# Optimization experiments

Measured on AMD Instinct MI355X. Metric: run time of the kernel, lower is better.

Reference implementation:

```python
import jax, jax.numpy as jnp
import numpy as np

D = 768
NH = 8
HD = D // NH
LAT = 64


def layernorm(x, g, b, eps=1e-5):
    mu = x.mean(-1, keepdims=True)
    var = ((x - mu) ** 2).mean(-1, keepdims=True)
    return (x - mu) * jax.lax.rsqrt(var + eps) * g + b


def mha(q, k, v, qw, qb, kw, kb, vw, vb, ow, ob):
    # torch nn.MultiheadAttention (batch_first): Linear is x @ W.T + b
    B, Lq, _ = q.shape
    qh = (q @ qw.T + qb).reshape(B, Lq, NH, HD)
    kh = (k @ kw.T + kb).reshape(B, -1, NH, HD)
    vh = (v @ vw.T + vb).reshape(B, -1, NH, HD)
    s = jnp.einsum('bqhd,bkhd->bhqk', qh, kh) * (1.0 / np.sqrt(HD))
    a = jax.nn.softmax(s, axis=-1)
    o = jnp.einsum('bhqk,bkhd->bqhd', a, vh).reshape(B, Lq, D)
    return o @ ow.T + ob


def setup_inputs() -> dict:
    key = jax.random.key(0)
    ks = jax.random.split(key, 16)
    w = lambda k, shape: (jax.random.normal(k, shape, jnp.float32) * 0.02)
    inp = {
        'frames': jax.random.normal(ks[0], (4, 4, 8, 3, 224, 224), jnp.float32),
        'pe_w': w(ks[1], (D, 3, 14, 14)), 'pe_b': jnp.zeros((D,), jnp.float32),
        'latents': jax.random.normal(ks[2], (LAT, D), jnp.float32),
        'ca_qw': w(ks[3], (D, D)), 'ca_qb': jnp.zeros((D,), jnp.float32),
        'ca_kw': w(ks[4], (D, D)), 'ca_kb': jnp.zeros((D,), jnp.float32),
        'ca_vw': w(ks[5], (D, D)), 'ca_vb': jnp.zeros((D,), jnp.float32),
        'ca_ow': w(ks[6], (D, D)), 'ca_ob': jnp.zeros((D,), jnp.float32),
        'nq_g': jnp.ones((D,), jnp.float32), 'nq_b': jnp.zeros((D,), jnp.float32),
        'nkv_g': jnp.ones((D,), jnp.float32), 'nkv_b': jnp.zeros((D,), jnp.float32),
        'no_g': jnp.ones((D,), jnp.float32), 'no_b': jnp.zeros((D,), jnp.float32),
        'm1_w': w(ks[7], (4 * D, D)), 'm1_b': jnp.zeros((4 * D,), jnp.float32),
        'm2_w': w(ks[8], (D, 4 * D)), 'm2_b': jnp.zeros((D,), jnp.float32),
        'sa_qw': w(ks[9], (D, D)), 'sa_qb': jnp.zeros((D,), jnp.float32),
        'sa_kw': w(ks[10], (D, D)), 'sa_kb': jnp.zeros((D,), jnp.float32),
        'sa_vw': w(ks[11], (D, D)), 'sa_vb': jnp.zeros((D,), jnp.float32),
        'sa_ow': w(ks[12], (D, D)), 'sa_ob': jnp.zeros((D,), jnp.float32),
        'f1_w': w(ks[13], (2 * D, D)), 'f1_b': jnp.zeros((2 * D,), jnp.float32),
        'f2_w': w(ks[14], (D, 2 * D)), 'f2_b': jnp.zeros((D,), jnp.float32),
        'n1_g': jnp.ones((D,), jnp.float32), 'n1_b': jnp.zeros((D,), jnp.float32),
        'n2_g': jnp.ones((D,), jnp.float32), 'n2_b': jnp.zeros((D,), jnp.float32),
    }
    return inp


def reference(frames, pe_w, pe_b, latents, ca_qw, ca_qb, ca_kw, ca_kb, ca_vw, ca_vb,
              ca_ow, ca_ob, nq_g, nq_b, nkv_g, nkv_b, no_g, no_b, m1_w, m1_b, m2_w, m2_b,
              sa_qw, sa_qb, sa_kw, sa_kb, sa_vw, sa_vb, sa_ow, sa_ob, f1_w, f1_b,
              f2_w, f2_b, n1_g, n1_b, n2_g, n2_b):
    B, S, T, C, H, W = frames.shape
    # --- patch embed (Conv2d k=14 s=14), batched over all seconds & frames ---
    f = frames.reshape(B * S * T, C, H, W)
    p = jax.lax.conv_general_dilated(
        f, pe_w, window_strides=(14, 14), padding='VALID',
        dimension_numbers=('NCHW', 'OIHW', 'NCHW')) + pe_b[None, :, None, None]
    npatch = p.shape[2] * p.shape[3]  # 256 patches per frame
    p = p.reshape(B * S * T, D, npatch).transpose(0, 2, 1)  # [BST, P, D]
    kv = p.reshape(B * S, T * npatch, D)  # per-second patch tokens
    # --- Perceiver second tokenizer (loop over seconds == batched over B*S) ---
    q = jnp.broadcast_to(latents[None], (B * S, LAT, D))
    out = mha(layernorm(q, nq_g, nq_b), layernorm(kv, nkv_g, nkv_b), kv,
              ca_qw, ca_qb, ca_kw, ca_kb, ca_vw, ca_vb, ca_ow, ca_ob)
    h = layernorm(out, no_g, no_b)
    tok = out + (jax.nn.gelu(h @ m1_w.T + m1_b) @ m2_w.T + m2_b)
    # concat second tokens along time
    x = tok.reshape(B, S * LAT, D)
    # --- temporal_agg: TransformerEncoderLayer (post-norm, relu, eval mode) ---
    attn = mha(x, x, x, sa_qw, sa_qb, sa_kw, sa_kb, sa_vw, sa_vb, sa_ow, sa_ob)
    x = layernorm(x + attn, n1_g, n1_b)
    ff = jax.nn.relu(x @ f1_w.T + f1_b) @ f2_w.T + f2_b
    x = layernorm(x + ff, n2_g, n2_b)
    return x
```

## Files before the change

kernel.cpp:

```cpp
#include <hip/hip_runtime.h>
#include <hip/hip_bf16.h>
#include <math.h>

typedef __hip_bfloat16 bf16;
typedef __attribute__((ext_vector_type(8))) short short8;
typedef __attribute__((ext_vector_type(4))) short short4v;
typedef __attribute__((ext_vector_type(4))) float f32x4;

__device__ __forceinline__ void gload16(const bf16* g, bf16* l) {
  __builtin_amdgcn_global_load_lds((const __attribute__((address_space(1))) void*)(g),
                                   (__attribute__((address_space(3))) void*)(l), 16, 0, 0);
}
__device__ __forceinline__ float bfu2f(unsigned short u) {
  union { unsigned u; float f; } c; c.u = ((unsigned)u) << 16; return c.f;
}
__device__ __forceinline__ short bf2s(float v) {
  union { bf16 h; short s; } c; c.h = __float2bfloat16(v); return c.s;
}
__device__ __forceinline__ short4v packbf4(f32x4 v) {
  short4v o;
  o[0] = bf2s(v[0]); o[1] = bf2s(v[1]); o[2] = bf2s(v[2]); o[3] = bf2s(v[3]);
  return o;
}

struct Seg { const float* src; bf16* dst; int rows, sc, dc; const float* scale; };
struct Segs { Seg s[13]; };

__global__ __launch_bounds__(256) void prepack_kernel(Segs segs) {
  Seg sg = segs.s[blockIdx.y];
  long long total = (long long)sg.rows * sg.dc;
  for (long long idx = (long long)blockIdx.x * 256 + threadIdx.x; idx < total;
       idx += (long long)gridDim.x * 256) {
    int r = (int)(idx / sg.dc), c = (int)(idx % sg.dc);
    float v = (c < sg.sc) ? sg.src[(long long)r * sg.sc + c] : 0.f;
    if (sg.scale && c < sg.sc) v *= sg.scale[c];
    sg.dst[idx] = __float2bfloat16(v);
  }
}

__global__ __launch_bounds__(256) void concat3_kernel(const float* __restrict__ a,
                                                      const float* __restrict__ b,
                                                      const float* __restrict__ c,
                                                      float* __restrict__ o) {
  int i = blockIdx.x * 256 + threadIdx.x;
  if (i < 2304)
    o[i] = i < 768 ? a[i] : (i < 1536 ? b[i - 768] : c[i - 1536]);
}

__global__ __launch_bounds__(256) void s12_kernel(const float* __restrict__ kw,
                                                  const float* __restrict__ g,
                                                  const float* __restrict__ b,
                                                  const float* __restrict__ kb,
                                                  float* __restrict__ s1,
                                                  float* __restrict__ s2) {
  int j = blockIdx.x;
  int tid = threadIdx.x;
  const float* wr_ = kw + (size_t)j * 768;
  float a = 0.f, c = 0.f;
  #pragma unroll
  for (int i = 0; i < 3; ++i) {
    int d = tid + i * 256;
    float wv = wr_[d];
    a += wv * g[d];
    c += wv * b[d];
  }
  __shared__ float red[16];
  for (int off = 32; off; off >>= 1) { a += __shfl_down(a, off); c += __shfl_down(c, off); }
  int w = tid >> 6;
  if ((tid & 63) == 0) { red[w] = a; red[8 + w] = c; }
  __syncthreads();
  if (tid == 0) {
    s1[j] = red[0] + red[1] + red[2] + red[3];
    s2[j] = red[8] + red[9] + red[10] + red[11] + kb[j];
  }
}

__global__ __launch_bounds__(256) void rowstats_kernel(const bf16* __restrict__ x,
                                                       float* __restrict__ mu,
                                                       float* __restrict__ rs) {
  int row = blockIdx.x * 4 + (threadIdx.x >> 6);
  int lane = threadIdx.x & 63;
  const unsigned short* p = (const unsigned short*)(x + (size_t)row * 768);
  float s = 0.f, sq = 0.f;
  #pragma unroll
  for (int i = 0; i < 3; ++i) {
    ushort4 v = *(const ushort4*)(p + lane * 4 + i * 256);
    float f0 = bfu2f(v.x), f1 = bfu2f(v.y), f2 = bfu2f(v.z), f3 = bfu2f(v.w);
    s += f0 + f1 + f2 + f3;
    sq += f0 * f0 + f1 * f1 + f2 * f2 + f3 * f3;
  }
  for (int off = 32; off; off >>= 1) { s += __shfl_down(s, off); sq += __shfl_down(sq, off); }
  if (lane == 0) {
    float m = s * (1.f / 768.f);
    float var = sq * (1.f / 768.f) - m * m;
    mu[row] = m;
    rs[row] = rsqrtf(var + 1e-5f);
  }
}

__global__ __launch_bounds__(256) void im2col_kernel(const float* __restrict__ frames,
                                                     bf16* __restrict__ out) {
  unsigned idx8 = blockIdx.x * 256u + threadIdx.x;
  unsigned m = idx8 / 76u;
  unsigned k0 = (idx8 % 76u) * 8u;
  unsigned n = m >> 8;
  unsigned p = m & 255u;
  unsigned py = p >> 4, px = p & 15u;
  const float* fb = frames + ((size_t)n * 3u) * 224u * 224u + (size_t)py * 14u * 224u +
                    px * 14u;
  short8 o;
  #pragma unroll
  for (int e = 0; e < 8; ++e) {
    unsigned k = k0 + e;
    float v = 0.f;
    if (k < 588u) {
      unsigned c = k / 196u, r = k % 196u;
      unsigned i = r / 14u, j = r % 14u;
      v = fb[((size_t)c * 224u + i) * 224u + j];
    }
    o[e] = bf2s(v);
  }
  *(short8*)(out + (size_t)m * 608u + k0) = o;
}

__global__ __launch_bounds__(256) void ln_kernel(const float* __restrict__ inF,
                                                 const bf16* __restrict__ inB,
                                                 const float* __restrict__ g,
                                                 const float* __restrict__ b,
                                                 float* __restrict__ outF,
                                                 bf16* __restrict__ outB,
                                                 int validRows) {
  int row = blockIdx.x;
  int tid = threadIdx.x;
  __shared__ float red[8];
  size_t base = (size_t)row * 768;
  if (row >= validRows) {
    for (int i = 0; i < 3; ++i) {
      int c = tid + i * 256;
      if (outB) outB[base + c] = __float2bfloat16(0.f);
      if (outF) outF[base + c] = 0.f;
    }
    return;
  }
  float x[3];
  for (int i = 0; i < 3; ++i) {
    int c = tid + i * 256;
    x[i] = inF ? inF[base + c] : __bfloat162float(inB[base + c]);
  }
  float s = x[0] + x[1] + x[2];
  float sq = x[0] * x[0] + x[1] * x[1] + x[2] * x[2];
  for (int off = 32; off; off >>= 1) {
    s += __shfl_down(s, off);
    sq += __shfl_down(sq, off);
  }
  int w = tid >> 6;
  if ((tid & 63) == 0) { red[w] = s; red[4 + w] = sq; }
  __syncthreads();
  if (tid == 0) {
    red[0] = red[0] + red[1] + red[2] + red[3];
    red[4] = red[4] + red[5] + red[6] + red[7];
  }
  __syncthreads();
  float mean = red[0] * (1.f / 768.f);
  float var = red[4] * (1.f / 768.f) - mean * mean;
  float rs = rsqrtf(var + 1e-5f);
  for (int i = 0; i < 3; ++i) {
    int c = tid + i * 256;
    float y = (x[i] - mean) * rs * g[c] + b[c];
    if (outF) outF[base + c] = y;
    if (outB) outB[base + c] = __float2bfloat16(y);
  }
}

__global__ __launch_bounds__(256) void gemm_bf16(
    const bf16* __restrict__ A, const bf16* __restrict__ Bw,
    const float* __restrict__ bias, const float* __restrict__ resid,
    float* __restrict__ outF, bf16* __restrict__ outB,
    int M, int N, int K, int act,
    const float* __restrict__ rowMu, const float* __restrict__ rowRs,
    const float* __restrict__ s1, const float* __restrict__ s2,
    bf16* __restrict__ outB2) {
  __shared__ __align__(16) bf16 As[2][4096];
  __shared__ __align__(16) bf16 Bs[2][4096];
  int tid = threadIdx.x;
  int nwg = gridDim.x * gridDim.y;
  int orig = blockIdx.y * gridDim.x + blockIdx.x;
  int xcd = orig & 7, loc = orig >> 3;
  int qq = nwg >> 3, rr = nwg & 7;
  int swz = (xcd < rr) ? (xcd * (qq + 1) + loc) : (rr * (qq + 1) + (xcd - rr) * qq + loc);
  int m0 = (swz / gridDim.x) * 128, n0 = (swz % gridDim.x) * 128;

  int lane = tid & 63, w = tid >> 6;
  int wr = w >> 1, wc = w & 1;
  int l15 = lane & 15, lq = lane >> 4;
  const bf16* Abase = A + (size_t)m0 * K + w * 8;
  const bf16* Bbase = Bw + (size_t)n0 * K + w * 8;
  f32x4 acc[4][4] = {};

  int nt = K >> 5;
  #pragma unroll
  for (int i = 0; i < 2; ++i) {
    int r = i * 64 + lane;
    gload16(Abase + (size_t)r * K, &As[0][(w * 2 + i) * 512]);
    gload16(Bbase + (size_t)r * K, &Bs[0][(w * 2 + i) * 512]);
  }
  for (int t = 0; t < nt; ++t) {
    int cur = t & 1;
    if (t + 1 < nt) {
      int kt = (t + 1) << 5;
      #pragma unroll
      for (int i = 0; i < 2; ++i) {
        int r = i * 64 + lane;
        gload16(Abase + (size_t)r * K + kt, &As[cur ^ 1][(w * 2 + i) * 512]);
        gload16(Bbase + (size_t)r * K + kt, &Bs[cur ^ 1][(w * 2 + i) * 512]);
      }
      asm volatile("s_waitcnt vmcnt(4)" ::: "memory");
    } else {
      asm volatile("s_waitcnt vmcnt(0)" ::: "memory");
    }
    __builtin_amdgcn_s_barrier();
    asm volatile("" ::: "memory");
    const bf16* Ab = &As[cur][lq * 1024];
    const bf16* Bb = &Bs[cur][lq * 1024];
    short8 af[4], bfr[4];
    #pragma unroll
    for (int mi = 0; mi < 4; ++mi)
      af[mi] = *(const short8*)(Ab + (wr * 64 + mi * 16 + l15) * 8);
    #pragma unroll
    for (int ni = 0; ni < 4; ++ni)
      bfr[ni] = *(const short8*)(Bb + (wc * 64 + ni * 16 + l15) * 8);
    __builtin_amdgcn_s_setprio(1);
    #pragma unroll
    for (int mi = 0; mi < 4; ++mi)
      #pragma unroll
      for (int ni = 0; ni < 4; ++ni)
        acc[mi][ni] = __builtin_amdgcn_mfma_f32_16x16x32_bf16(bfr[ni], af[mi],
                                                              acc[mi][ni], 0, 0, 0);
    __builtin_amdgcn_s_setprio(0);
    asm volatile("" ::: "memory");
    __builtin_amdgcn_s_barrier();
  }

  if (act == 3) {
    #pragma unroll
    for (int ni = 0; ni < 4; ++ni) {
      int c0 = n0 + wc * 64 + ni * 16 + lq * 4;
      if (c0 < 768) {
        f32x4 bv = *(const f32x4*)(bias + c0);
        #pragma unroll
        for (int mi = 0; mi < 4; ++mi) {
          int row = m0 + wr * 64 + mi * 16 + l15;
          f32x4 v = acc[mi][ni] + bv;
          *(short4v*)(outB + (size_t)row * 768 + c0) = packbf4(v);
        }
      } else {
        int ck = c0 - 768;
        f32x4 a1 = *(const f32x4*)(s1 + ck);
        f32x4 a2 = *(const f32x4*)(s2 + ck);
        #pragma unroll
        for (int mi = 0; mi < 4; ++mi) {
          int row = m0 + wr * 64 + mi * 16 + l15;
          float rs_ = rowRs[row], mu_ = rowMu[row];
          f32x4 v;
          #pragma unroll
          for (int j = 0; j < 4; ++j) v[j] = rs_ * (acc[mi][ni][j] - mu_ * a1[j]) + a2[j];
          *(short4v*)(outB2 + (size_t)row * 768 + ck) = packbf4(v);
        }
      }
    }
    return;
  }

  #pragma unroll
  for (int ni = 0; ni < 4; ++ni) {
    int c0 = n0 + wc * 64 + ni * 16 + lq * 4;
    f32x4 bv = {};
    if (bias) bv = *(const f32x4*)(bias + c0);
    #pragma unroll
    for (int mi = 0; mi < 4; ++mi) {
      int row = m0 + wr * 64 + mi * 16 + l15;
      f32x4 v = acc[mi][ni] + bv;
      if (act == 1) {
        #pragma unroll
        for (int j = 0; j < 4; ++j) {
          float x = v[j];
          v[j] = 0.5f * x * (1.f + tanhf(0.79788456080286535f * (x + 0.044715f * x * x * x)));
        }
      } else if (act == 2) {
        #pragma unroll
        for (int j = 0; j < 4; ++j) v[j] = fmaxf(v[j], 0.f);
      }
      size_t idx = (size_t)row * N + c0;
      if (resid) v += *(const f32x4*)(resid + idx);
      if (outF) *(f32x4*)(outF + idx) = v;
      if (outB) *(short4v*)(outB + idx) = packbf4(v);
    }
  }
}

__global__ __launch_bounds__(256) void flash_kernel(
    const bf16* __restrict__ Q, const bf16* __restrict__ Kp,
    const bf16* __restrict__ V, bf16* __restrict__ O,
    int Lk, int qRPB, int kRPB, int oRPB, int ld) {
  const float scale = 0.10206207261596575f;
  __shared__ bf16 Vt[96 * 72];
  __shared__ bf16 Ps[4 * 16 * 72];
  int tid = threadIdx.x, lane = tid & 63, w = tid >> 6;
  int l15 = lane & 15, lq = lane >> 4;
  int b = blockIdx.z, h = blockIdx.y, qt = blockIdx.x;
  int qbase = b * qRPB + qt * 64 + w * 16;
  int kbase = b * kRPB;
  int obase = b * oRPB + qt * 64 + w * 16;
  int ch = h * 96;

  short8 aQ[3];
  #pragma unroll
  for (int kd = 0; kd < 3; ++kd)
    aQ[kd] = *(const short8*)(Q + (size_t)(qbase + l15) * ld + ch + kd * 32 + lq * 8);

  f32x4 oacc[6] = {};
  float mrun[4] = {-1e30f, -1e30f, -1e30f, -1e30f};
  float lrun[4] = {0.f, 0.f, 0.f, 0.f};

  for (int kc = 0; kc < Lk; kc += 64) {
    for (int u = tid; u < 768; u += 256) {
      int kk = u / 12, dc = u % 12;
      short8 v = *(const short8*)(V + (size_t)(kbase + kc + kk) * ld + ch + dc * 8);
      const bf16* pv = (const bf16*)&v;
      #pragma unroll
      for (int e = 0; e < 8; ++e) Vt[(dc * 8 + e) * 72 + kk] = pv[e];
    }
    __syncthreads();

    f32x4 sacc[4] = {};
    #pragma unroll
    for (int ni = 0; ni < 4; ++ni)
      #pragma unroll
      for (int kd = 0; kd < 3; ++kd) {
        short8 bK = *(const short8*)(Kp + (size_t)(kbase + kc + ni * 16 + l15) * ld +
                                     ch + kd * 32 + lq * 8);
        sacc[ni] = __builtin_amdgcn_mfma_f32_16x16x32_bf16(aQ[kd], bK, sacc[ni], 0, 0, 0);
      }
    #pragma unroll
    for (int ni = 0; ni < 4; ++ni)
      #pragma unroll
      for (int j = 0; j < 4; ++j) sacc[ni][j] *= scale;

    float al[4];
    #pragma unroll
    for (int j = 0; j < 4; ++j) {
      float mx = fmaxf(fmaxf(sacc[0][j], sacc[1][j]), fmaxf(sacc[2][j], sacc[3][j]));
      #pragma unroll
      for (int off = 1; off < 16; off <<= 1) mx = fmaxf(mx, __shfl_xor(mx, off));
      float mnew = fmaxf(mrun[j], mx);
      float alpha = __expf(mrun[j] - mnew);
      float rsum = 0.f;
      #pragma unroll
      for (int ni = 0; ni < 4; ++ni) {
        float p = __expf(sacc[ni][j] - mnew);
        sacc[ni][j] = p;
        rsum += p;
      }
      #pragma unroll
      for (int off = 1; off < 16; off <<= 1) rsum += __shfl_xor(rsum, off);
      lrun[j] = lrun[j] * alpha + rsum;
      mrun[j] = mnew;
      al[j] = alpha;
    }

    #pragma unroll
    for (int ni = 0; ni < 4; ++ni)
      #pragma unroll
      for (int j = 0; j < 4; ++j)
        Ps[(w * 16 + lq * 4 + j) * 72 + ni * 16 + l15] = __float2bfloat16(sacc[ni][j]);
    #pragma unroll
    for (int t = 0; t < 6; ++t)
      #pragma unroll
      for (int j = 0; j < 4; ++j) oacc[t][j] *= al[j];
    short8 aP[2];
    #pragma unroll
    for (int ks = 0; ks < 2; ++ks)
      aP[ks] = *(const short8*)(&Ps[(w * 16 + l15) * 72 + ks * 32 + lq * 8]);
    #pragma unroll
    for (int t = 0; t < 6; ++t)
      #pragma unroll
      for (int ks = 0; ks < 2; ++ks) {
        short8 bV = *(const short8*)(&Vt[(t * 16 + l15) * 72 + ks * 32 + lq * 8]);
        oacc[t] = __builtin_amdgcn_mfma_f32_16x16x32_bf16(aP[ks], bV, oacc[t], 0, 0, 0);
      }
    __syncthreads();
  }

  #pragma unroll
  for (int t = 0; t < 6; ++t)
    #pragma unroll
    for (int j = 0; j < 4; ++j) {
      int row = obase + lq * 4 + j;
      int col = ch + t * 16 + l15;
      O[(size_t)row * 768 + col] = __float2bfloat16(oacc[t][j] / lrun[j]);
    }
}

__global__ __launch_bounds__(256) void flash_split_kernel(
    const bf16* __restrict__ Q, const bf16* __restrict__ Kp,
    const bf16* __restrict__ V, float* __restrict__ Opart,
    float* __restrict__ Mpart, float* __restrict__ Lpart,
    int splitLen, int kRPB) {
  const float scale = 0.10206207261596575f;
  __shared__ bf16 Vt[96 * 72];
  __shared__ bf16 Ps[4 * 16 * 72];
  int tid = threadIdx.x, lane = tid & 63, w = tid >> 6;
  int l15 = lane & 15, lq = lane >> 4;
  int s = blockIdx.x, h = blockIdx.y, b = blockIdx.z;
  int kbase = b * kRPB + s * splitLen;
  int ch = h * 96;

  short8 aQ[3];
  #pragma unroll
  for (int kd = 0; kd < 3; ++kd)
    aQ[kd] = *(const short8*)(Q + (size_t)(w * 16 + l15) * 768 + ch + kd * 32 + lq * 8);

  f32x4 oacc[6] = {};
  float mrun[4] = {-1e30f, -1e30f, -1e30f, -1e30f};
  float lrun[4] = {0.f, 0.f, 0.f, 0.f};

  for (int kc = 0; kc < splitLen; kc += 64) {
    for (int u = tid; u < 768; u += 256) {
      int kk = u / 12, dc = u % 12;
      short8 v = *(const short8*)(V + (size_t)(kbase + kc + kk) * 768 + ch + dc * 8);
      const bf16* pv = (const bf16*)&v;
      #pragma unroll
      for (int e = 0; e < 8; ++e) Vt[(dc * 8 + e) * 72 + kk] = pv[e];
    }
    __syncthreads();

    f32x4 sacc[4] = {};
    #pragma unroll
    for (int ni = 0; ni < 4; ++ni)
      #pragma unroll
      for (int kd = 0; kd < 3; ++kd) {
        short8 bK = *(const short8*)(Kp + (size_t)(kbase + kc + ni * 16 + l15) * 768 +
                                     ch + kd * 32 + lq * 8);
        sacc[ni] = __builtin_amdgcn_mfma_f32_16x16x32_bf16(aQ[kd], bK, sacc[ni], 0, 0, 0);
      }
    #pragma unroll
    for (int ni = 0; ni < 4; ++ni)
      #pragma unroll
      for (int j = 0; j < 4; ++j) sacc[ni][j] *= scale;

    float al[4];
    #pragma unroll
    for (int j = 0; j < 4; ++j) {
      float mx = fmaxf(fmaxf(sacc[0][j], sacc[1][j]), fmaxf(sacc[2][j], sacc[3][j]));
      #pragma unroll
      for (int off = 1; off < 16; off <<= 1) mx = fmaxf(mx, __shfl_xor(mx, off));
      float mnew = fmaxf(mrun[j], mx);
      float alpha = __expf(mrun[j] - mnew);
      float rsum = 0.f;
      #pragma unroll
      for (int ni = 0; ni < 4; ++ni) {
        float p = __expf(sacc[ni][j] - mnew);
        sacc[ni][j] = p;
        rsum += p;
      }
      #pragma unroll
      for (int off = 1; off < 16; off <<= 1) rsum += __shfl_xor(rsum, off);
      lrun[j] = lrun[j] * alpha + rsum;
      mrun[j] = mnew;
      al[j] = alpha;
    }

    #pragma unroll
    for (int ni = 0; ni < 4; ++ni)
      #pragma unroll
      for (int j = 0; j < 4; ++j)
        Ps[(w * 16 + lq * 4 + j) * 72 + ni * 16 + l15] = __float2bfloat16(sacc[ni][j]);
    #pragma unroll
    for (int t = 0; t < 6; ++t)
      #pragma unroll
      for (int j = 0; j < 4; ++j) oacc[t][j] *= al[j];
    short8 aP[2];
    #pragma unroll
    for (int ks = 0; ks < 2; ++ks)
      aP[ks] = *(const short8*)(&Ps[(w * 16 + l15) * 72 + ks * 32 + lq * 8]);
    #pragma unroll
    for (int t = 0; t < 6; ++t)
      #pragma unroll
      for (int ks = 0; ks < 2; ++ks) {
        short8 bV = *(const short8*)(&Vt[(t * 16 + l15) * 72 + ks * 32 + lq * 8]);
        oacc[t] = __builtin_amdgcn_mfma_f32_16x16x32_bf16(aP[ks], bV, oacc[t], 0, 0, 0);
      }
    __syncthreads();
  }

  int orow = b * 64 + w * 16;
  #pragma unroll
  for (int t = 0; t < 6; ++t)
    #pragma unroll
    for (int j = 0; j < 4; ++j)
      Opart[(size_t)(s * 1024 + orow + lq * 4 + j) * 768 + ch + t * 16 + l15] = oacc[t][j];
  if (l15 == 0) {
    #pragma unroll
    for (int j = 0; j < 4; ++j) {
      int qqi = w * 16 + lq * 4 + j;
      int mi = ((s * 16 + b) * 8 + h) * 64 + qqi;
      Mpart[mi] = mrun[j];
      Lpart[mi] = lrun[j];
    }
  }
}

__global__ __launch_bounds__(256) void flash_merge_kernel(
    const float* __restrict__ Opart, const float* __restrict__ Mpart,
    const float* __restrict__ Lpart, bf16* __restrict__ O, int nsplit) {
  int row = blockIdx.x;
  int tid = threadIdx.x;
  int c0 = tid * 3;
  int b = row >> 6, q = row & 63;
  int h = c0 / 96;
  float m = -1e30f;
  for (int s = 0; s < nsplit; ++s)
    m = fmaxf(m, Mpart[((s * 16 + b) * 8 + h) * 64 + q]);
  float l = 0.f, o0 = 0.f, o1 = 0.f, o2 = 0.f;
  for (int s = 0; s < nsplit; ++s) {
    int mi = ((s * 16 + b) * 8 + h) * 64 + q;
    float ws = __expf(Mpart[mi] - m);
    l += ws * Lpart[mi];
    const float* op = Opart + (size_t)(s * 1024 + row) * 768 + c0;
    o0 += ws * op[0]; o1 += ws * op[1]; o2 += ws * op[2];
  }
  float inv = 1.f / l;
  size_t ob = (size_t)row * 768 + c0;
  O[ob]     = __float2bfloat16(o0 * inv);
  O[ob + 1] = __float2bfloat16(o1 * inv);
  O[ob + 2] = __float2bfloat16(o2 * inv);
}

extern "C" void kernel_launch(void* const* d_in, const int* in_sizes, int n_in,
                              void* d_out, int out_size, void* d_ws, size_t ws_size,
                              hipStream_t stream) {
  const float* frames = (const float*)d_in[0];
  const float* pe_w   = (const float*)d_in[1];
  const float* pe_b   = (const float*)d_in[2];
  const float* latents= (const float*)d_in[3];
  const float* ca_qw  = (const float*)d_in[4];  const float* ca_qb = (const float*)d_in[5];
  const float* ca_kw  = (const float*)d_in[6];  const float* ca_kb = (const float*)d_in[7];
  const float* ca_vw  = (const float*)d_in[8];  const float* ca_vb = (const float*)d_in[9];
  const float* ca_ow  = (const float*)d_in[10]; const float* ca_ob = (const float*)d_in[11];
  const float* nq_g   = (const float*)d_in[12]; const float* nq_b  = (const float*)d_in[13];
  const float* nkv_g  = (const float*)d_in[14]; const float* nkv_b = (const float*)d_in[15];
  const float* no_g   = (const float*)d_in[16]; const float* no_b  = (const float*)d_in[17];
  const float* m1_w   = (const float*)d_in[18]; const float* m1_b  = (const float*)d_in[19];
  const float* m2_w   = (const float*)d_in[20]; const float* m2_b  = (const float*)d_in[21];
  const float* sa_qw  = (const float*)d_in[22]; const float* sa_qb = (const float*)d_in[23];
  const float* sa_kw  = (const float*)d_in[24]; const float* sa_kb = (const float*)d_in[25];
  const float* sa_vw  = (const float*)d_in[26]; const float* sa_vb = (const float*)d_in[27];
  const float* sa_ow  = (const float*)d_in[28]; const float* sa_ob = (const float*)d_in[29];
  const float* f1_w   = (const float*)d_in[30]; const float* f1_b  = (const float*)d_in[31];
  const float* f2_w   = (const float*)d_in[32]; const float* f2_b  = (const float*)d_in[33];
  const float* n1_g   = (const float*)d_in[34]; const float* n1_b  = (const float*)d_in[35];
  const float* n2_g   = (const float*)d_in[36]; const float* n2_b  = (const float*)d_in[37];

  char* ws = (char*)d_ws;
  size_t off = 0;
  auto take = [&](size_t bytes) -> char* {
    char* p = ws + off;
    off += (bytes + 255) & ~(size_t)255;
    return p;
  };

  bf16* w_pe   = (bf16*)take((size_t)768 * 608 * 2);
  bf16* w_caq  = (bf16*)take((size_t)768 * 768 * 2);
  bf16* w_cakv = (bf16*)take((size_t)1536 * 768 * 2);
  bf16* w_cao  = (bf16*)take((size_t)768 * 768 * 2);
  bf16* w_m1   = (bf16*)take((size_t)3072 * 768 * 2);
  bf16* w_m2   = (bf16*)take((size_t)768 * 3072 * 2);
  bf16* w_saq  = (bf16*)take((size_t)768 * 768 * 2);
  bf16* w_sak  = (bf16*)take((size_t)768 * 768 * 2);
  bf16* w_sav  = (bf16*)take((size_t)768 * 768 * 2);
  bf16* w_sao  = (bf16*)take((size_t)768 * 768 * 2);
  bf16* w_f1   = (bf16*)take((size_t)1536 * 768 * 2);
  bf16* w_f2   = (bf16*)take((size_t)768 * 1536 * 2);
  float* sab_cat = (float*)take((size_t)2304 * 4);
  float* s1v  = (float*)take((size_t)768 * 4);
  float* s2v  = (float*)take((size_t)768 * 4);
  float* muv  = (float*)take((size_t)32768 * 4);
  float* rsv  = (float*)take((size_t)32768 * 4);

  bf16* q_ln = (bf16*)take((size_t)128 * 768 * 2);
  bf16* qh   = (bf16*)take((size_t)128 * 768 * 2);

  bf16* kv = (bf16*)take((size_t)32768 * 768 * 2);
  bf16* vh = (bf16*)take((size_t)32768 * 768 * 2);
  bf16* kh = (bf16*)take((size_t)32768 * 768 * 2);

  const size_t REGION = (size_t)32768 * 608 * 2;
  char* region = take(REGION);
  bf16*  imcol = (bf16*)region;
  float* Opart = (float*)region;
  float* Mpart = (float*)(region + 25165824);
  float* Lpart = (float*)(region + 25165824 + 262144);
  bf16*  attn_o = (bf16*)(region + REGION - (size_t)1024 * 768 * 2);
  size_t ro = 0;
  auto rtake = [&](size_t bytes) -> char* {
    char* p = region + ro;
    ro += (bytes + 255) & ~(size_t)255;
    return p;
  };
  float* out_f  = (float*)rtake((size_t)1024 * 768 * 4);
  bf16*  h_b    = (bf16*)rtake((size_t)1024 * 768 * 2);
  bf16*  g_b    = (bf16*)rtake((size_t)1024 * 3072 * 2);
  float* tok_f  = (float*)rtake((size_t)1024 * 768 * 4);
  bf16*  tok_b  = (bf16*)rtake((size_t)1024 * 768 * 2);
  bf16*  xqkv   = (bf16*)rtake((size_t)1024 * 2304 * 2);
  bf16*  sa_o   = (bf16*)rtake((size_t)1024 * 768 * 2);
  float* y_f    = (float*)rtake((size_t)1024 * 768 * 4);
  float* x1f    = (float*)rtake((size_t)1024 * 768 * 4);
  bf16*  x1b    = (bf16*)rtake((size_t)1024 * 768 * 2);
  bf16*  ff1    = (bf16*)rtake((size_t)1024 * 1536 * 2);
  float* z_f    = (float*)rtake((size_t)1024 * 768 * 4);
  (void)ws_size; (void)in_sizes; (void)n_in; (void)out_size;

  Segs segs;
  segs.s[0]  = {pe_w,  w_pe,  768, 588, 608, nullptr};
  segs.s[1]  = {ca_qw, w_caq, 768, 768, 768, nullptr};
  segs.s[2]  = {ca_vw, w_cakv, 768, 768, 768, nullptr};
  segs.s[3]  = {ca_kw, w_cakv + (size_t)768 * 768, 768, 768, 768, nkv_g};
  segs.s[4]  = {ca_ow, w_cao, 768, 768, 768, nullptr};
  segs.s[5]  = {m1_w,  w_m1,  3072, 768, 768, nullptr};
  segs.s[6]  = {m2_w,  w_m2,  768, 3072, 3072, nullptr};
  segs.s[7]  = {sa_qw, w_saq, 768, 768, 768, nullptr};
  segs.s[8]  = {sa_kw, w_sak, 768, 768, 768, nullptr};
  segs.s[9]  = {sa_vw, w_sav, 768, 768, 768, nullptr};
  segs.s[10] = {f1_w,  w_f1,  1536, 768, 768, nullptr};
  segs.s[11] = {f2_w,  w_f2,  768, 1536, 1536, nullptr};
  segs.s[12] = {sa_ow, w_sao, 768, 768, 768, nullptr};
  prepack_kernel<<<dim3(2304, 13), 256, 0, stream>>>(segs);
  concat3_kernel<<<9, 256, 0, stream>>>(sa_qb, sa_kb, sa_vb, sab_cat);
  s12_kernel<<<768, 256, 0, stream>>>(ca_kw, nkv_g, nkv_b, ca_kb, s1v, s2v);

  ln_kernel<<<128, 256, 0, stream>>>(latents, nullptr, nq_g, nq_b, nullptr, q_ln, 64);

  im2col_kernel<<<9728, 256, 0, stream>>>(frames, imcol);

  gemm_bf16<<<dim3(6, 256), 256, 0, stream>>>(imcol, w_pe, pe_b, nullptr, nullptr, kv,
                                              32768, 768, 608, 0,
                                              nullptr, nullptr, nullptr, nullptr, nullptr);

  gemm_bf16<<<dim3(6, 1), 256, 0, stream>>>(q_ln, w_caq, ca_qb, nullptr, nullptr, qh,
                                            128, 768, 768, 0,
                                            nullptr, nullptr, nullptr, nullptr, nullptr);

  rowstats_kernel<<<8192, 256, 0, stream>>>(kv, muv, rsv);

  gemm_bf16<<<dim3(12, 256), 256, 0, stream>>>(kv, w_cakv, ca_vb, nullptr, nullptr, vh,
                                               32768, 1536, 768, 3,
                                               muv, rsv, s1v, s2v, kh);

  flash_split_kernel<<<dim3(8, 8, 16), 256, 0, stream>>>(qh, kh, vh, Opart, Mpart, Lpart,
                                                         256, 2048);
  flash_merge_kernel<<<1024, 256, 0, stream>>>(Opart, Mpart, Lpart, attn_o, 8);

  gemm_bf16<<<dim3(6, 8), 256, 0, stream>>>(attn_o, w_cao, ca_ob, nullptr, out_f, nullptr,
                                            1024, 768, 768, 0,
                                            nullptr, nullptr, nullptr, nullptr, nullptr);

  ln_kernel<<<1024, 256, 0, stream>>>(out_f, nullptr, no_g, no_b, nullptr, h_b, 1024);

  gemm_bf16<<<dim3(24, 8), 256, 0, stream>>>(h_b, w_m1, m1_b, nullptr, nullptr, g_b,
                                             1024, 3072, 768, 1,
                                             nullptr, nullptr, nullptr, nullptr, nullptr);

  gemm_bf16<<<dim3(6, 8), 256, 0, stream>>>(g_b, w_m2, m2_b, out_f, tok_f, tok_b,
                                            1024, 768, 3072, 0,
                                            nullptr, nullptr, nullptr, nullptr, nullptr);

  gemm_bf16<<<dim3(18, 8), 256, 0, stream>>>(tok_b, w_saq, sab_cat, nullptr, nullptr, xqkv,
                                             1024, 2304, 768, 0,
                                             nullptr, nullptr, nullptr, nullptr, nullptr);

  flash_kernel<<<dim3(4, 8, 4), 256, 0, stream>>>(xqkv, xqkv + 768, xqkv + 1536, sa_o,
                                                  256, 256, 256, 256, 2304);

  gemm_bf16<<<dim3(6, 8), 256, 0, stream>>>(sa_o, w_sao, sa_ob, tok_f, y_f, nullptr,
                                            1024, 768, 768, 0,
                                            nullptr, nullptr, nullptr, nullptr, nullptr);

  ln_kernel<<<1024, 256, 0, stream>>>(y_f, nullptr, n1_g, n1_b, x1f, x1b, 1024);

  gemm_bf16<<<dim3(12, 8), 256, 0, stream>>>(x1b, w_f1, f1_b, nullptr, nullptr, ff1,
                                             1024, 1536, 768, 2,
                                             nullptr, nullptr, nullptr, nullptr, nullptr);

  gemm_bf16<<<dim3(6, 8), 256, 0, stream>>>(ff1, w_f2, f2_b, x1f, z_f, nullptr,
                                            1024, 768, 1536, 0,
                                            nullptr, nullptr, nullptr, nullptr, nullptr);

  ln_kernel<<<1024, 256, 0, stream>>>(z_f, nullptr, n2_g, n2_b, (float*)d_out, nullptr, 1024);
}
```

Before: 761.9 us.

## Add 256x256-tile 512-thread GEMM for the two large patch/KV projections

Introduces a new gemm256 kernel with 256x256 output tiles, 8 waves, BK=64 and double-buffered direct global-to-LDS loads. It is used for the patch-embedding GEMM and the fused K/V projection, which are the two 32768-row GEMMs. The patch K dimension is padded from 608 to 640 so it divides by 64, and the im2col buffer is moved to alias the vh/kh buffer. Larger tiles raise arithmetic intensity and cut A/B reloads. In exchange the kernel uses 128 KB of LDS and many accumulator registers, which limits occupancy and leaves fewer workgroups (384 and 768) to fill the CUs.

```diff
diff --git a/kernel.cpp b/kernel.cpp
--- a/kernel.cpp
+++ b/kernel.cpp
@@ -101,8 +101,8 @@
 __global__ __launch_bounds__(256) void im2col_kernel(const float* __restrict__ frames,
                                                      bf16* __restrict__ out) {
   unsigned idx8 = blockIdx.x * 256u + threadIdx.x;
-  unsigned m = idx8 / 76u;
-  unsigned k0 = (idx8 % 76u) * 8u;
+  unsigned m = idx8 / 80u;
+  unsigned k0 = (idx8 % 80u) * 8u;
   unsigned n = m >> 8;
   unsigned p = m & 255u;
   unsigned py = p >> 4, px = p & 15u;
@@ -120,7 +120,7 @@
     }
     o[e] = bf2s(v);
   }
-  *(short8*)(out + (size_t)m * 608u + k0) = o;
+  *(short8*)(out + (size_t)m * 640u + k0) = o;
 }
 
 __global__ __launch_bounds__(256) void ln_kernel(const float* __restrict__ inF,
@@ -172,14 +172,126 @@
   }
 }
 
+__global__ __launch_bounds__(512, 2) void gemm256(
+    const bf16* __restrict__ A, const bf16* __restrict__ Bw,
+    const float* __restrict__ bias,
+    bf16* __restrict__ outB,
+    int M, int N, int K, int act,
+    const float* __restrict__ rowMu, const float* __restrict__ rowRs,
+    const float* __restrict__ s1, const float* __restrict__ s2,
+    bf16* __restrict__ outB2) {
+  __shared__ __align__(16) bf16 As[2][16384];
+  __shared__ __align__(16) bf16 Bs[2][16384];
+  int tid = threadIdx.x;
+  int nwg = gridDim.x * gridDim.y;
+  int orig = blockIdx.y * gridDim.x + blockIdx.x;
+  int xcd = orig & 7, loc = orig >> 3;
+  int qq = nwg >> 3, rr = nwg & 7;
+  int swz = (xcd < rr) ? (xcd * (qq + 1) + loc) : (rr * (qq + 1) + (xcd - rr) * qq + loc);
+  int m0 = (swz / gridDim.x) * 256, n0 = (swz % gridDim.x) * 256;
+
+  int lane = tid & 63, w = tid >> 6;
+  int wr = w >> 2, wc = w & 3;
+  int l15 = lane & 15, lq = lane >> 4;
+
+  f32x4 acc[8][4] = {};
+
+  #define STAGE256(buf, kt)                                                     \
+    {                                                                           \
+      _Pragma("unroll")                                                         \
+      for (int i = 0; i < 4; ++i) {                                             \
+        int r = w * 4 + i;                                                      \
+        int koct = r >> 2, row0 = (r & 3) * 64;                                 \
+        gload16(A + (size_t)(m0 + row0 + lane) * K + (kt) + koct * 8,           \
+                &As[buf][r * 512]);                                             \
+        gload16(Bw + (size_t)(n0 + row0 + lane) * K + (kt) + koct * 8,          \
+                &Bs[buf][r * 512]);                                             \
+      }                                                                         \
+    }
+
+  int nt = K >> 6;
+  STAGE256(0, 0);
+  for (int t = 0; t < nt; ++t) {
+    int cur = t & 1;
+    if (t + 1 < nt) {
+      STAGE256(cur ^ 1, (t + 1) << 6);
+      asm volatile("s_waitcnt vmcnt(8)" ::: "memory");
+    } else {
+      asm volatile("s_waitcnt vmcnt(0)" ::: "memory");
+    }
+    __builtin_amdgcn_s_barrier();
+    asm volatile("" ::: "memory");
+    #pragma unroll
+    for (int ks = 0; ks < 2; ++ks) {
+      int koct = ks * 4 + lq;
+      short8 af[8], bfr[4];
+      #pragma unroll
+      for (int mi = 0; mi < 8; ++mi)
+        af[mi] = *(const short8*)(&As[cur][(koct * 256 + wr * 128 + mi * 16 + l15) * 8]);
+      #pragma unroll
+      for (int ni = 0; ni < 4; ++ni)
+        bfr[ni] = *(const short8*)(&Bs[cur][(koct * 256 + wc * 64 + ni * 16 + l15) * 8]);
+      #pragma unroll
+      for (int mi = 0; mi < 8; ++mi)
+        #pragma unroll
+        for (int ni = 0; ni < 4; ++ni)
+          acc[mi][ni] = __builtin_amdgcn_mfma_f32_16x16x32_bf16(bfr[ni], af[mi],
+                                                                acc[mi][ni], 0, 0, 0);
+    }
+    asm volatile("" ::: "memory");
+    __builtin_amdgcn_s_barrier();
+  }
+  #undef STAGE256
+
+  if (act == 3) {
+    #pragma unroll
+    for (int ni = 0; ni < 4; ++ni) {
+      int c0 = n0 + wc * 64 + ni * 16 + lq * 4;
+      if (c0 < 768) {
+        f32x4 bv = *(const f32x4*)(bias + c0);
+        #pragma unroll
+        for (int mi = 0; mi < 8; ++mi) {
+          int row = m0 + wr * 128 + mi * 16 + l15;
+          f32x4 v = acc[mi][ni] + bv;
+          *(short4v*)(outB + (size_t)row * 768 + c0) = packbf4(v);
+        }
+      } else {
+        int ck = c0 - 768;
+        f32x4 a1 = *(const f32x4*)(s1 + ck);
+        f32x4 a2 = *(const f32x4*)(s2 + ck);
+        #pragma unroll
+        for (int mi = 0; mi < 8; ++mi) {
+          int row = m0 + wr * 128 + mi * 16 + l15;
+          float rs_ = rowRs[row], mu_ = rowMu[row];
+          f32x4 v;
+          #pragma unroll
+          for (int j = 0; j < 4; ++j) v[j] = rs_ * (acc[mi][ni][j] - mu_ * a1[j]) + a2[j];
+          *(short4v*)(outB2 + (size_t)row * 768 + ck) = packbf4(v);
+        }
+      }
+    }
+    return;
+  }
+
+  #pragma unroll
+  for (int ni = 0; ni < 4; ++ni) {
+    int c0 = n0 + wc * 64 + ni * 16 + lq * 4;
+    f32x4 bv = {};
+    if (bias) bv = *(const f32x4*)(bias + c0);
+    #pragma unroll
+    for (int mi = 0; mi < 8; ++mi) {
+      int row = m0 + wr * 128 + mi * 16 + l15;
+      f32x4 v = acc[mi][ni] + bv;
+      *(short4v*)(outB + (size_t)row * N + c0) = packbf4(v);
+    }
+  }
+}
+
 __global__ __launch_bounds__(256) void gemm_bf16(
     const bf16* __restrict__ A, const bf16* __restrict__ Bw,
     const float* __restrict__ bias, const float* __restrict__ resid,
     float* __restrict__ outF, bf16* __restrict__ outB,
-    int M, int N, int K, int act,
-    const float* __restrict__ rowMu, const float* __restrict__ rowRs,
-    const float* __restrict__ s1, const float* __restrict__ s2,
-    bf16* __restrict__ outB2) {
+    int M, int N, int K, int act) {
   __shared__ __align__(16) bf16 As[2][4096];
   __shared__ __align__(16) bf16 Bs[2][4096];
   int tid = threadIdx.x;
@@ -239,36 +351,6 @@
     __builtin_amdgcn_s_setprio(0);
     asm volatile("" ::: "memory");
     __builtin_amdgcn_s_barrier();
-  }
-
-  if (act == 3) {
-    #pragma unroll
-    for (int ni = 0; ni < 4; ++ni) {
-      int c0 = n0 + wc * 64 + ni * 16 + lq * 4;
-      if (c0 < 768) {
-        f32x4 bv = *(const f32x4*)(bias + c0);
-        #pragma unroll
-        for (int mi = 0; mi < 4; ++mi) {
-          int row = m0 + wr * 64 + mi * 16 + l15;
-          f32x4 v = acc[mi][ni] + bv;
-          *(short4v*)(outB + (size_t)row * 768 + c0) = packbf4(v);
-        }
-      } else {
-        int ck = c0 - 768;
-        f32x4 a1 = *(const f32x4*)(s1 + ck);
-        f32x4 a2 = *(const f32x4*)(s2 + ck);
-        #pragma unroll
-        for (int mi = 0; mi < 4; ++mi) {
-          int row = m0 + wr * 64 + mi * 16 + l15;
-          float rs_ = rowRs[row], mu_ = rowMu[row];
-          f32x4 v;
-          #pragma unroll
-          for (int j = 0; j < 4; ++j) v[j] = rs_ * (acc[mi][ni][j] - mu_ * a1[j]) + a2[j];
-          *(short4v*)(outB2 + (size_t)row * 768 + ck) = packbf4(v);
-        }
-      }
-    }
-    return;
   }
 
   #pragma unroll
@@ -569,7 +651,7 @@
     return p;
   };
 
-  bf16* w_pe   = (bf16*)take((size_t)768 * 608 * 2);
+  bf16* w_pe   = (bf16*)take((size_t)768 * 640 * 2);
   bf16* w_caq  = (bf16*)take((size_t)768 * 768 * 2);
   bf16* w_cakv = (bf16*)take((size_t)1536 * 768 * 2);
   bf16* w_cao  = (bf16*)take((size_t)768 * 768 * 2);
@@ -590,13 +672,14 @@
   bf16* q_ln = (bf16*)take((size_t)128 * 768 * 2);
   bf16* qh   = (bf16*)take((size_t)128 * 768 * 2);
 
-  bf16* kv = (bf16*)take((size_t)32768 * 768 * 2);
-  bf16* vh = (bf16*)take((size_t)32768 * 768 * 2);
-  bf16* kh = (bf16*)take((size_t)32768 * 768 * 2);
+  bf16* kv   = (bf16*)take((size_t)32768 * 768 * 2);
+  bf16* vhkh = (bf16*)take((size_t)2 * 32768 * 768 * 2);
+  bf16* vh = vhkh;
+  bf16* kh = vhkh + (size_t)32768 * 768;
+  bf16* imcol = vhkh;
 
   const size_t REGION = (size_t)32768 * 608 * 2;
   char* region = take(REGION);
-  bf16*  imcol = (bf16*)region;
   float* Opart = (float*)region;
   float* Mpart = (float*)(region + 25165824);
   float* Lpart = (float*)(region + 25165824 + 262144);
@@ -622,7 +705,7 @@
   (void)ws_size; (void)in_sizes; (void)n_in; (void)out_size;
 
   Segs segs;
-  segs.s[0]  = {pe_w,  w_pe,  768, 588, 608, nullptr};
+  segs.s[0]  = {pe_w,  w_pe,  768, 588, 640, nullptr};
   segs.s[1]  = {ca_qw, w_caq, 768, 768, 768, nullptr};
   segs.s[2]  = {ca_vw, w_cakv, 768, 768, 768, nullptr};
   segs.s[3]  = {ca_kw, w_cakv + (size_t)768 * 768, 768, 768, 768, nkv_g};
@@ -641,60 +724,52 @@
 
   ln_kernel<<<128, 256, 0, stream>>>(latents, nullptr, nq_g, nq_b, nullptr, q_ln, 64);
 
-  im2col_kernel<<<9728, 256, 0, stream>>>(frames, imcol);
-
-  gemm_bf16<<<dim3(6, 256), 256, 0, stream>>>(imcol, w_pe, pe_b, nullptr, nullptr, kv,
-                                              32768, 768, 608, 0,
-                                              nullptr, nullptr, nullptr, nullptr, nullptr);
+  im2col_kernel<<<10240, 256, 0, stream>>>(frames, imcol);
+
+  gemm256<<<dim3(3, 128), 512, 0, stream>>>(imcol, w_pe, pe_b, kv,
+                                            32768, 768, 640, 0,
+                                            nullptr, nullptr, nullptr, nullptr, nullptr);
 
   gemm_bf16<<<dim3(6, 1), 256, 0, stream>>>(q_ln, w_caq, ca_qb, nullptr, nullptr, qh,
-                                            128, 768, 768, 0,
-                                            nullptr, nullptr, nullptr, nullptr, nullptr);
+                                            128, 768, 768, 0);
 
   rowstats_kernel<<<8192, 256, 0, stream>>>(kv, muv, rsv);
 
-  gemm_bf16<<<dim3(12, 256), 256, 0, stream>>>(kv, w_cakv, ca_vb, nullptr, nullptr, vh,
-                                               32768, 1536, 768, 3,
-                                               muv, rsv, s1v, s2v, kh);
+  gemm256<<<dim3(6, 128), 512, 0, stream>>>(kv, w_cakv, ca_vb, vh,
+                                            32768, 1536, 768, 3,
+                                            muv, rsv, s1v, s2v, kh);
 
   flash_split_kernel<<<dim3(8, 8, 16), 256, 0, stream>>>(qh, kh, vh, Opart, Mpart, Lpart,
                                                          256, 2048);
   flash_merge_kernel<<<1024, 256, 0, stream>>>(Opart, Mpart, Lpart, attn_o, 8);
 
   gemm_bf16<<<dim3(6, 8), 256, 0, stream>>>(attn_o, w_cao, ca_ob, nullptr, out_f, nullptr,
-                                            1024, 768, 768, 0,
-                                            nullptr, nullptr, nullptr, nullptr, nullptr);
+                                            1024, 768, 768, 0);
 
   ln_kernel<<<1024, 256, 0, stream>>>(out_f, nullptr, no_g, no_b, nullptr, h_b, 1024);
 
   gemm_bf16<<<dim3(24, 8), 256, 0, stream>>>(h_b, w_m1, m1_b, nullptr, nullptr, g_b,
-                                             1024, 3072, 768, 1,
-                                             nullptr, nullptr, nullptr, nullptr, nullptr);
+                                             1024, 3072, 768, 1);
 
   gemm_bf16<<<dim3(6, 8), 256, 0, stream>>>(g_b, w_m2, m2_b, out_f, tok_f, tok_b,
-                                            1024, 768, 3072, 0,
-                                            nullptr, nullptr, nullptr, nullptr, nullptr);
+                                            1024, 768, 3072, 0);
 
   gemm_bf16<<<dim3(18, 8), 256, 0, stream>>>(tok_b, w_saq, sab_cat, nullptr, nullptr, xqkv,
-                                             1024, 2304, 768, 0,
-                                             nullptr, nullptr, nullptr, nullptr, nullptr);
+                                             1024, 2304, 768, 0);
 
   flash_kernel<<<dim3(4, 8, 4), 256, 0, stream>>>(xqkv, xqkv + 768, xqkv + 1536, sa_o,
                                                   256, 256, 256, 256, 2304);
 
   gemm_bf16<<<dim3(6, 8), 256, 0, stream>>>(sa_o, w_sao, sa_ob, tok_f, y_f, nullptr,
-                                            1024, 768, 768, 0,
-                                            nullptr, nullptr, nullptr, nullptr, nullptr);
+                                            1024, 768, 768, 0);
 
   ln_kernel<<<1024, 256, 0, stream>>>(y_f, nullptr, n1_g, n1_b, x1f, x1b, 1024);
 
   gemm_bf16<<<dim3(12, 8), 256, 0, stream>>>(x1b, w_f1, f1_b, nullptr, nullptr, ff1,
-                                             1024, 1536, 768, 2,
-                                             nullptr, nullptr, nullptr, nullptr, nullptr);
+                                             1024, 1536, 768, 2);
 
   gemm_bf16<<<dim3(6, 8), 256, 0, stream>>>(ff1, w_f2, f2_b, x1f, z_f, nullptr,
-                                            1024, 768, 1536, 0,
-                                            nullptr, nullptr, nullptr, nullptr, nullptr);
+                                            1024, 768, 1536, 0);
 
   ln_kernel<<<1024, 256, 0, stream>>>(z_f, nullptr, n2_g, n2_b, (float*)d_out, nullptr, 1024);
 }
```

Result: no change. 747.9 us (-1.8%).
